# Optimization experiments

Hardware: AMD Instinct MI355X
Metric: run time of the kernel (lower is better)

The kernel has to match this reference:

```python
import jax, jax.numpy as jnp
import numpy as np

N, IN_FT, OUT_FT = 10000, 512, 256


def setup_inputs() -> dict:
    key = jax.random.key(0)
    k1, k2, k3 = jax.random.split(key, 3)
    feat = jax.random.normal(k1, (N, IN_FT), dtype=jnp.float32)
    adj = jax.random.uniform(k2, (N, N), dtype=jnp.float32)  # nonneg edge weights
    W = jax.random.normal(k3, (IN_FT, OUT_FT), dtype=jnp.float32) * 0.05
    conv_bias = jnp.zeros((OUT_FT,), dtype=jnp.float32)
    extra_bias = jnp.zeros((OUT_FT,), dtype=jnp.float32)
    return {"feat": feat, "adj": adj, "W": W,
            "conv_bias": conv_bias, "extra_bias": extra_bias}


def reference(feat, adj, W, conv_bias, extra_bias):
    n = adj.shape[0]
    idx = jnp.arange(n)
    # gcn_norm: fill_diag(adj, 1.0) -> self loops with weight 1 on the diagonal
    A_hat = adj.at[idx, idx].set(1.0)  # [N, N]
    deg = A_hat.sum(axis=1)            # row degree
    dinv = jnp.where(deg > 0, jax.lax.rsqrt(deg), 0.0)  # D^-1/2
    # linear transform first (standard GCNConv order), then normalized aggregation
    h = feat @ W                                   # [N, OUT_FT]
    # D^-1/2 A_hat D^-1/2 h, fused as row/col scalings to avoid a second NxN buffer
    agg = dinv[:, None] * (A_hat @ (dinv[:, None] * h))
    out = agg + conv_bias + extra_bias
    return jax.nn.relu(out)
```

## Files before the change

### kernel.cpp

```cpp
#include <hip/hip_runtime.h>

#define NROW 10000
#define NF 256
#define KF 512
#define MP 10048
#define NTILES 157

typedef __attribute__((ext_vector_type(8))) short short8x;
typedef __attribute__((ext_vector_type(4))) float f32x4;

__device__ __forceinline__ unsigned int bf16rne(float f){
  unsigned int u = __builtin_bit_cast(unsigned int, f);
  u += 0x7fffu + ((u >> 16) & 1u);
  return u >> 16;
}

__global__ void k_zero(float4* __restrict__ p){
  p[blockIdx.x * 256 + threadIdx.x] = make_float4(0.f, 0.f, 0.f, 0.f);
}

__global__ __launch_bounds__(256) void k_deg2(const float* __restrict__ adj,
        float* __restrict__ degp){
  int t = threadIdx.x;
  int lane = t & 63;
  int row = blockIdx.x * 4 + (t >> 6);
  const f32x4* src = (const f32x4*)(adj + (size_t)row * NROW);
  const f32x4 zero4 = {0.f, 0.f, 0.f, 0.f};
  f32x4 acc0 = zero4, acc1 = zero4;
  f32x4 v[8];
  #pragma unroll
  for (int it = 0; it < 4; ++it){
    int base = it * 512 + lane;
    #pragma unroll
    for (int b = 0; b < 8; ++b) v[b] = src[base + b * 64];
    #pragma unroll
    for (int b = 0; b < 4; ++b){ acc0 += v[2*b]; acc1 += v[2*b + 1]; }
  }
  {
    int base = 2048 + lane;
    #pragma unroll
    for (int b = 0; b < 8; ++b){
      int fi = base + b * 64;
      v[b] = (fi < 2500) ? src[fi] : zero4;
    }
    #pragma unroll
    for (int b = 0; b < 4; ++b){ acc0 += v[2*b]; acc1 += v[2*b + 1]; }
  }
  f32x4 a = acc0 + acc1;
  float s = (a[0] + a[1]) + (a[2] + a[3]);
  #pragma unroll
  for (int off = 32; off; off >>= 1) s += __shfl_down(s, off);
  if (lane == 0) degp[row] = s;
}

__global__ void k_dinv(const float* __restrict__ degp, const float* __restrict__ adj,
                       float* __restrict__ dinv, unsigned short* __restrict__ hsT){
  int i = blockIdx.x * 256 + threadIdx.x;
  if (i >= MP) return;
  float d = 0.f;
  if (i < NROW){
    float tot = degp[i] + 1.0f - adj[(size_t)i * NROW + i];
    d = tot > 0.f ? rsqrtf(tot) : 0.f;
  }
  dinv[i] = d;
  if (i < NF){
    unsigned int* tz = (unsigned int*)(hsT + (size_t)i * MP + NROW);
    #pragma unroll
    for (int m = 0; m < (MP - NROW) / 2; ++m) tz[m] = 0u;
  }
}

__global__ __launch_bounds__(128) void k_featw(const float* __restrict__ feat,
        const float* __restrict__ W, const float* __restrict__ dinv,
        unsigned short* __restrict__ hsT){
  __shared__ __align__(16) float fs[8][512];
  int t = threadIdx.x;
  int i0 = blockIdx.x * 8;
  #pragma unroll
  for (int it = 0; it < 8; ++it){
    int idx = it * 128 + t;
    int r = idx >> 7, c4 = (idx & 127) * 4;
    *(float4*)&fs[r][c4] = *(const float4*)(feat + (size_t)(i0 + r) * KF + c4);
  }
  __syncthreads();
  float acc[8][2];
  #pragma unroll
  for (int r = 0; r < 8; ++r){ acc[r][0] = 0.f; acc[r][1] = 0.f; }
  int c0 = t, c1 = t + 128;
  for (int k = 0; k < KF; k += 4){
    const float* Wk = W + (size_t)k * NF;
    float w0a = Wk[c0],        w0b = Wk[c1];
    float w1a = Wk[NF + c0],   w1b = Wk[NF + c1];
    float w2a = Wk[2*NF + c0], w2b = Wk[2*NF + c1];
    float w3a = Wk[3*NF + c0], w3b = Wk[3*NF + c1];
    #pragma unroll
    for (int r = 0; r < 8; ++r){
      float4 f = *(const float4*)&fs[r][k];
      float a0 = acc[r][0], a1 = acc[r][1];
      a0 = fmaf(f.x, w0a, a0); a1 = fmaf(f.x, w0b, a1);
      a0 = fmaf(f.y, w1a, a0); a1 = fmaf(f.y, w1b, a1);
      a0 = fmaf(f.z, w2a, a0); a1 = fmaf(f.z, w2b, a1);
      a0 = fmaf(f.w, w3a, a0); a1 = fmaf(f.w, w3b, a1);
      acc[r][0] = a0; acc[r][1] = a1;
    }
  }
  float dv[8];
  #pragma unroll
  for (int r = 0; r < 8; ++r) dv[r] = dinv[i0 + r];
  unsigned short* d0 = hsT + (size_t)c0 * MP + i0;
  unsigned short* d1 = hsT + (size_t)c1 * MP + i0;
  #pragma unroll
  for (int r = 0; r < 8; r += 2){
    unsigned int u0 = bf16rne(acc[r][0] * dv[r]) | (bf16rne(acc[r+1][0] * dv[r+1]) << 16);
    unsigned int u1 = bf16rne(acc[r][1] * dv[r]) | (bf16rne(acc[r+1][1] * dv[r+1]) << 16);
    *(unsigned int*)(d0 + r) = u0;
    *(unsigned int*)(d1 + r) = u1;
  }
}

__global__ __launch_bounds__(256, 2) void k_gemm(const float* __restrict__ adj,
        const unsigned short* __restrict__ hsT, float* __restrict__ out){
  __shared__ __align__(16) unsigned short Al[64][72];
  __shared__ __align__(16) unsigned short Bl[256][72];
  int t = threadIdx.x;
  int lane = t & 63, wid = t >> 6;
  int wr = wid >> 1, wc = wid & 1;
  int r0 = blockIdx.x * 64;
  int by = blockIdx.y;
  int kt0 = by * 39 + (by > 0 ? 1 : 0);
  int kt1 = (by + 1) * 39 + 1;

  f32x4 acc[2][8];
  #pragma unroll
  for (int a = 0; a < 2; ++a)
    #pragma unroll
    for (int b = 0; b < 8; ++b)
      #pragma unroll
      for (int j = 0; j < 4; ++j) acc[a][b][j] = 0.f;

  int arow = t >> 4;
  int acol = (t & 15) * 4;
  int bcol = t >> 3;
  int bko  = (t & 7) * 8;

  for (int kt = kt0; kt < kt1; ++kt){
    int k0 = kt * 64;
    #pragma unroll
    for (int it = 0; it < 4; ++it){
      int row = it * 16 + arow;
      int gr  = r0 + row;
      int gcb = k0 + acol;
      int er = gr  < NROW      ? gr  : NROW - 1;
      int ec = gcb <= NROW - 4 ? gcb : NROW - 4;
      float4 v = *(const float4*)(adj + (size_t)er * NROW + ec);
      float f0 = v.x, f1 = v.y, f2 = v.z, f3 = v.w;
      if (gr == gcb    ) f0 = 1.f;
      if (gr == gcb + 1) f1 = 1.f;
      if (gr == gcb + 2) f2 = 1.f;
      if (gr == gcb + 3) f3 = 1.f;
      unsigned int u0 = bf16rne(f0) | (bf16rne(f1) << 16);
      unsigned int u1 = bf16rne(f2) | (bf16rne(f3) << 16);
      *(uint2*)&Al[row][acol] = make_uint2(u0, u1);
    }
    #pragma unroll
    for (int it = 0; it < 8; ++it){
      int cc = it * 32 + bcol;
      *(uint4*)&Bl[cc][bko] = *(const uint4*)(hsT + (size_t)cc * MP + k0 + bko);
    }
    __syncthreads();
    #pragma unroll
    for (int kk = 0; kk < 64; kk += 32){
      short8x a0 = *(const short8x*)&Al[wr*32      + (lane & 15)][kk + (lane >> 4) * 8];
      short8x a1 = *(const short8x*)&Al[wr*32 + 16 + (lane & 15)][kk + (lane >> 4) * 8];
      #pragma unroll
      for (int ni = 0; ni < 8; ++ni){
        short8x b = *(const short8x*)&Bl[wc*128 + ni*16 + (lane & 15)][kk + (lane >> 4) * 8];
        acc[0][ni] = __builtin_amdgcn_mfma_f32_16x16x32_bf16(a0, b, acc[0][ni], 0, 0, 0);
        acc[1][ni] = __builtin_amdgcn_mfma_f32_16x16x32_bf16(a1, b, acc[1][ni], 0, 0, 0);
      }
    }
    __syncthreads();
  }
  #pragma unroll
  for (int mi = 0; mi < 2; ++mi){
    #pragma unroll
    for (int ni = 0; ni < 8; ++ni){
      int gc = wc*128 + ni*16 + (lane & 15);
      #pragma unroll
      for (int j = 0; j < 4; ++j){
        int gr = r0 + wr*32 + mi*16 + (lane >> 4) * 4 + j;
        if (gr < NROW) atomicAdd(out + (size_t)gr * NF + gc, acc[mi][ni][j]);
      }
    }
  }
}

__global__ void k_epi(float* __restrict__ out, const float* __restrict__ dinv,
                      const float* __restrict__ cb, const float* __restrict__ eb){
  int e = (blockIdx.x * 256 + threadIdx.x) * 4;
  int i = e >> 8, c = e & 255;
  float di = dinv[i];
  float4 v = *(float4*)(out + e);
  v.x = fmaxf(fmaf(v.x, di, cb[c+0] + eb[c+0]), 0.f);
  v.y = fmaxf(fmaf(v.y, di, cb[c+1] + eb[c+1]), 0.f);
  v.z = fmaxf(fmaf(v.z, di, cb[c+2] + eb[c+2]), 0.f);
  v.w = fmaxf(fmaf(v.w, di, cb[c+3] + eb[c+3]), 0.f);
  *(float4*)(out + e) = v;
}

extern "C" void kernel_launch(void* const* d_in, const int* in_sizes, int n_in,
                              void* d_out, int out_size, void* d_ws, size_t ws_size,
                              hipStream_t stream){
  const float* feat = (const float*)d_in[0];
  const float* adj  = (const float*)d_in[1];
  const float* W    = (const float*)d_in[2];
  const float* cb   = (const float*)d_in[3];
  const float* eb   = (const float*)d_in[4];
  float* out = (float*)d_out;

  float* degp = (float*)d_ws;
  float* dinv = (float*)((char*)d_ws + (256u << 10));
  unsigned short* hsT = (unsigned short*)((char*)d_ws + (512u << 10));

  k_zero <<<(NROW*NF)/1024,   256, 0, stream>>>((float4*)out);
  k_deg2 <<<NROW/4,           256, 0, stream>>>(adj, degp);
  k_dinv <<<(MP + 255)/256,   256, 0, stream>>>(degp, adj, dinv, hsT);
  k_featw<<<NROW/8,           128, 0, stream>>>(feat, W, dinv, hsT);
  k_gemm <<<dim3(NTILES, 4),  256, 0, stream>>>(adj, hsT, out);
  k_epi  <<<(NROW*NF)/1024,   256, 0, stream>>>(out, dinv, cb, eb);
}
```

Baseline: 279.0 us.

## Drop B shared-memory staging, read hsT directly from global with wider K tiles

The GEMM kernel no longer stages the transposed h tile in LDS. Each lane loads its bf16 B fragments straight from global/L2, and only the adjacency tile is staged, now 256 wide in K per iteration instead of 64. This cuts LDS traffic and halves the number of barriers per K element, and the smaller LDS footprint plus launch_bounds 4 allow more resident blocks. In exchange, B fragments are re-read from cache by every wave, and the padded K length grows to 10240, which adds extra zero work.

```diff
diff --git a/kernel.cpp b/kernel.cpp
--- a/kernel.cpp
+++ b/kernel.cpp
@@ -3,7 +3,8 @@
 #define NROW 10000
 #define NF 256
 #define KF 512
-#define MP 10048
+#define MPK 10240
+#define NKT 40
 #define NTILES 157
 
 typedef __attribute__((ext_vector_type(8))) short short8x;
@@ -56,17 +57,17 @@
 __global__ void k_dinv(const float* __restrict__ degp, const float* __restrict__ adj,
                        float* __restrict__ dinv, unsigned short* __restrict__ hsT){
   int i = blockIdx.x * 256 + threadIdx.x;
-  if (i >= MP) return;
+  if (i >= MPK) return;
   float d = 0.f;
   if (i < NROW){
     float tot = degp[i] + 1.0f - adj[(size_t)i * NROW + i];
     d = tot > 0.f ? rsqrtf(tot) : 0.f;
   }
-  dinv[i] = d;
+  if (i < MPK) dinv[i] = d;
   if (i < NF){
-    unsigned int* tz = (unsigned int*)(hsT + (size_t)i * MP + NROW);
-    #pragma unroll
-    for (int m = 0; m < (MP - NROW) / 2; ++m) tz[m] = 0u;
+    unsigned int* tz = (unsigned int*)(hsT + (size_t)i * MPK + NROW);
+    #pragma unroll
+    for (int m = 0; m < (MPK - NROW) / 2; ++m) tz[m] = 0u;
   }
 }
 
@@ -107,8 +108,8 @@
   float dv[8];
   #pragma unroll
   for (int r = 0; r < 8; ++r) dv[r] = dinv[i0 + r];
-  unsigned short* d0 = hsT + (size_t)c0 * MP + i0;
-  unsigned short* d1 = hsT + (size_t)c1 * MP + i0;
+  unsigned short* d0 = hsT + (size_t)c0 * MPK + i0;
+  unsigned short* d1 = hsT + (size_t)c1 * MPK + i0;
   #pragma unroll
   for (int r = 0; r < 8; r += 2){
     unsigned int u0 = bf16rne(acc[r][0] * dv[r]) | (bf16rne(acc[r+1][0] * dv[r+1]) << 16);
@@ -118,17 +119,16 @@
   }
 }
 
-__global__ __launch_bounds__(256, 2) void k_gemm(const float* __restrict__ adj,
+__global__ __launch_bounds__(256, 4) void k_gemm(const float* __restrict__ adj,
         const unsigned short* __restrict__ hsT, float* __restrict__ out){
-  __shared__ __align__(16) unsigned short Al[64][72];
-  __shared__ __align__(16) unsigned short Bl[256][72];
+  __shared__ __align__(16) unsigned short Al[64][264];
   int t = threadIdx.x;
   int lane = t & 63, wid = t >> 6;
   int wr = wid >> 1, wc = wid & 1;
+  int l15 = lane & 15, hi = lane >> 4;
   int r0 = blockIdx.x * 64;
-  int by = blockIdx.y;
-  int kt0 = by * 39 + (by > 0 ? 1 : 0);
-  int kt1 = (by + 1) * 39 + 1;
+  int kt0 = blockIdx.y * (NKT/4);
+  int kt1 = kt0 + (NKT/4);
 
   f32x4 acc[2][8];
   #pragma unroll
@@ -138,43 +138,42 @@
       #pragma unroll
       for (int j = 0; j < 4; ++j) acc[a][b][j] = 0.f;
 
-  int arow = t >> 4;
-  int acol = (t & 15) * 4;
-  int bcol = t >> 3;
-  int bko  = (t & 7) * 8;
+  int srow = t >> 4;
+  int scol = (t & 15) * 4;
+  const unsigned short* bbase = hsT + (size_t)(wc*128 + l15) * MPK;
 
   for (int kt = kt0; kt < kt1; ++kt){
-    int k0 = kt * 64;
+    int k0 = kt * 256;
     #pragma unroll
     for (int it = 0; it < 4; ++it){
-      int row = it * 16 + arow;
+      int row = it * 16 + srow;
       int gr  = r0 + row;
-      int gcb = k0 + acol;
-      int er = gr  < NROW      ? gr  : NROW - 1;
-      int ec = gcb <= NROW - 4 ? gcb : NROW - 4;
-      float4 v = *(const float4*)(adj + (size_t)er * NROW + ec);
-      float f0 = v.x, f1 = v.y, f2 = v.z, f3 = v.w;
-      if (gr == gcb    ) f0 = 1.f;
-      if (gr == gcb + 1) f1 = 1.f;
-      if (gr == gcb + 2) f2 = 1.f;
-      if (gr == gcb + 3) f3 = 1.f;
-      unsigned int u0 = bf16rne(f0) | (bf16rne(f1) << 16);
-      unsigned int u1 = bf16rne(f2) | (bf16rne(f3) << 16);
-      *(uint2*)&Al[row][acol] = make_uint2(u0, u1);
-    }
-    #pragma unroll
-    for (int it = 0; it < 8; ++it){
-      int cc = it * 32 + bcol;
-      *(uint4*)&Bl[cc][bko] = *(const uint4*)(hsT + (size_t)cc * MP + k0 + bko);
+      int er  = gr < NROW ? gr : NROW - 1;
+      const float* rowp = adj + (size_t)er * NROW;
+      #pragma unroll
+      for (int j = 0; j < 4; ++j){
+        int gcb = k0 + scol + j * 64;
+        int ec  = gcb <= NROW - 4 ? gcb : NROW - 4;
+        float4 v = *(const float4*)(rowp + ec);
+        float f0 = v.x, f1 = v.y, f2 = v.z, f3 = v.w;
+        if (gr == gcb    ) f0 = 1.f;
+        if (gr == gcb + 1) f1 = 1.f;
+        if (gr == gcb + 2) f2 = 1.f;
+        if (gr == gcb + 3) f3 = 1.f;
+        unsigned int u0 = bf16rne(f0) | (bf16rne(f1) << 16);
+        unsigned int u1 = bf16rne(f2) | (bf16rne(f3) << 16);
+        *(uint2*)&Al[row][scol + j * 64] = make_uint2(u0, u1);
+      }
     }
     __syncthreads();
     #pragma unroll
-    for (int kk = 0; kk < 64; kk += 32){
-      short8x a0 = *(const short8x*)&Al[wr*32      + (lane & 15)][kk + (lane >> 4) * 8];
-      short8x a1 = *(const short8x*)&Al[wr*32 + 16 + (lane & 15)][kk + (lane >> 4) * 8];
+    for (int k8 = 0; k8 < 8; ++k8){
+      short8x a0 = *(const short8x*)&Al[wr*32      + l15][k8*32 + hi*8];
+      short8x a1 = *(const short8x*)&Al[wr*32 + 16 + l15][k8*32 + hi*8];
+      const unsigned short* bk = bbase + k0 + k8*32 + hi*8;
       #pragma unroll
       for (int ni = 0; ni < 8; ++ni){
-        short8x b = *(const short8x*)&Bl[wc*128 + ni*16 + (lane & 15)][kk + (lane >> 4) * 8];
+        short8x b = *(const short8x*)(bk + (size_t)ni * 16 * MPK);
         acc[0][ni] = __builtin_amdgcn_mfma_f32_16x16x32_bf16(a0, b, acc[0][ni], 0, 0, 0);
         acc[1][ni] = __builtin_amdgcn_mfma_f32_16x16x32_bf16(a1, b, acc[1][ni], 0, 0, 0);
       }
@@ -185,10 +184,10 @@
   for (int mi = 0; mi < 2; ++mi){
     #pragma unroll
     for (int ni = 0; ni < 8; ++ni){
-      int gc = wc*128 + ni*16 + (lane & 15);
+      int gc = wc*128 + ni*16 + l15;
       #pragma unroll
       for (int j = 0; j < 4; ++j){
-        int gr = r0 + wr*32 + mi*16 + (lane >> 4) * 4 + j;
+        int gr = r0 + wr*32 + mi*16 + hi*4 + j;
         if (gr < NROW) atomicAdd(out + (size_t)gr * NF + gc, acc[mi][ni][j]);
       }
     }
@@ -224,7 +223,7 @@
 
   k_zero <<<(NROW*NF)/1024,   256, 0, stream>>>((float4*)out);
   k_deg2 <<<NROW/4,           256, 0, stream>>>(adj, degp);
-  k_dinv <<<(MP + 255)/256,   256, 0, stream>>>(degp, adj, dinv, hsT);
+  k_dinv <<<(MPK + 255)/256,  256, 0, stream>>>(degp, adj, dinv, hsT);
   k_featw<<<NROW/8,           128, 0, stream>>>(feat, W, dinv, hsT);
   k_gemm <<<dim3(NTILES, 4),  256, 0, stream>>>(adj, hsT, out);
   k_epi  <<<(NROW*NF)/1024,   256, 0, stream>>>(out, dinv, cb, eb);
```

Result: slower. 470.4 us (+68.6%).

## Double-buffer adj tiles via direct global-to-LDS loads and replace atomics with split-K partials

Applied to the files above, without the earlier changes.

The GEMM kernel now streams fp32 adjacency tiles straight into swizzled LDS with global_load_lds, double-buffered so the next tile loads while the current one is computed. The bf16 conversion moves to fragment-read time, and the per-element diagonal fix-up is dropped from the inner loop. The epilogue instead adds the self-loop correction (1 - a_ii)·h_i. Atomic adds into a zeroed output are replaced by four split-K partial buffers that the epilogue sums, which also removes the zero kernel. This costs extra workspace traffic for the partials and doubles the LDS footprint for A.

```diff
diff --git a/kernel.cpp b/kernel.cpp
--- a/kernel.cpp
+++ b/kernel.cpp
@@ -4,6 +4,7 @@
 #define NF 256
 #define KF 512
 #define MP 10048
+#define NKT 157
 #define NTILES 157
 
 typedef __attribute__((ext_vector_type(8))) short short8x;
@@ -14,9 +15,14 @@
   u += 0x7fffu + ((u >> 16) & 1u);
   return u >> 16;
 }
-
-__global__ void k_zero(float4* __restrict__ p){
-  p[blockIdx.x * 256 + threadIdx.x] = make_float4(0.f, 0.f, 0.f, 0.f);
+__device__ __forceinline__ float bf2f(unsigned short h){
+  unsigned int u = ((unsigned int)h) << 16;
+  return __builtin_bit_cast(float, u);
+}
+__device__ __forceinline__ void gload16(const void* g, void* l){
+  __builtin_amdgcn_global_load_lds(
+      (const __attribute__((address_space(1))) unsigned int*)g,
+      (__attribute__((address_space(3))) unsigned int*)l, 16, 0, 0);
 }
 
 __global__ __launch_bounds__(256) void k_deg2(const float* __restrict__ adj,
@@ -119,16 +125,18 @@
 }
 
 __global__ __launch_bounds__(256, 2) void k_gemm(const float* __restrict__ adj,
-        const unsigned short* __restrict__ hsT, float* __restrict__ out){
-  __shared__ __align__(16) unsigned short Al[64][72];
+        const unsigned short* __restrict__ hsT, float* __restrict__ part){
+  __shared__ __align__(16) float Afs[2][4096];
   __shared__ __align__(16) unsigned short Bl[256][72];
   int t = threadIdx.x;
   int lane = t & 63, wid = t >> 6;
   int wr = wid >> 1, wc = wid & 1;
+  int l15 = lane & 15, hi = lane >> 4;
   int r0 = blockIdx.x * 64;
   int by = blockIdx.y;
   int kt0 = by * 39 + (by > 0 ? 1 : 0);
   int kt1 = (by + 1) * 39 + 1;
+  int ktf = kt1 < NKT ? kt1 : NKT - 1;
 
   f32x4 acc[2][8];
   #pragma unroll
@@ -138,74 +146,145 @@
       #pragma unroll
       for (int j = 0; j < 4; ++j) acc[a][b][j] = 0.f;
 
-  int arow = t >> 4;
-  int acol = (t & 15) * 4;
+  const float* asrc[4];
+  int adstoff[4];
+  {
+    int srow = (wid << 2) + hi;
+    #pragma unroll
+    for (int j = 0; j < 4; ++j){
+      int row = j * 16 + srow;
+      int gr  = r0 + row;
+      int er  = gr < NROW ? gr : NROW - 1;
+      int logf = ((l15 * 16) ^ ((row & 7) << 4)) >> 2;
+      asrc[j] = adj + (size_t)er * NROW + logf;
+      adstoff[j] = (j * 4096 + wid * 1024 + lane * 16) >> 2;
+    }
+  }
   int bcol = t >> 3;
   int bko  = (t & 7) * 8;
 
-  for (int kt = kt0; kt < kt1; ++kt){
+  #define STAGE_A(buf, k0g) { \
+    _Pragma("unroll") \
+    for (int j = 0; j < 4; ++j) \
+      gload16(asrc[j] + (k0g), &Afs[buf][adstoff[j]]); }
+
+  #define LDA_FRAG(dst, buf, rowv, kk) { \
+    int row_ = (rowv); \
+    int sw_  = (row_ & 7) << 4; \
+    const char* rp_ = (const char*)&Afs[buf][row_ * 64]; \
+    int b0_ = (kk) * 128 + hi * 32; \
+    f32x4 lo_ = *(const f32x4*)(rp_ + ((b0_     ) ^ sw_)); \
+    f32x4 hh_ = *(const f32x4*)(rp_ + ((b0_ + 16) ^ sw_)); \
+    union { unsigned int u[4]; short8x s; } cv_; \
+    cv_.u[0] = bf16rne(lo_[0]) | (bf16rne(lo_[1]) << 16); \
+    cv_.u[1] = bf16rne(lo_[2]) | (bf16rne(lo_[3]) << 16); \
+    cv_.u[2] = bf16rne(hh_[0]) | (bf16rne(hh_[1]) << 16); \
+    cv_.u[3] = bf16rne(hh_[2]) | (bf16rne(hh_[3]) << 16); \
+    dst = cv_.s; }
+
+  #define COMPUTE(buf) { \
+    _Pragma("unroll") \
+    for (int kk = 0; kk < 2; ++kk){ \
+      short8x a0_, a1_; \
+      LDA_FRAG(a0_, buf, wr*32      + l15, kk); \
+      LDA_FRAG(a1_, buf, wr*32 + 16 + l15, kk); \
+      _Pragma("unroll") \
+      for (int ni = 0; ni < 8; ++ni){ \
+        short8x b_ = *(const short8x*)&Bl[wc*128 + ni*16 + l15][kk*32 + hi*8]; \
+        acc[0][ni] = __builtin_amdgcn_mfma_f32_16x16x32_bf16(a0_, b_, acc[0][ni], 0, 0, 0); \
+        acc[1][ni] = __builtin_amdgcn_mfma_f32_16x16x32_bf16(a1_, b_, acc[1][ni], 0, 0, 0); \
+      } \
+    } }
+
+  int cur = 0;
+  STAGE_A(0, kt0 * 64);
+  for (int kt = kt0; kt < ktf; ++kt){
     int k0 = kt * 64;
-    #pragma unroll
-    for (int it = 0; it < 4; ++it){
-      int row = it * 16 + arow;
-      int gr  = r0 + row;
-      int gcb = k0 + acol;
-      int er = gr  < NROW      ? gr  : NROW - 1;
-      int ec = gcb <= NROW - 4 ? gcb : NROW - 4;
-      float4 v = *(const float4*)(adj + (size_t)er * NROW + ec);
-      float f0 = v.x, f1 = v.y, f2 = v.z, f3 = v.w;
-      if (gr == gcb    ) f0 = 1.f;
-      if (gr == gcb + 1) f1 = 1.f;
-      if (gr == gcb + 2) f2 = 1.f;
-      if (gr == gcb + 3) f3 = 1.f;
-      unsigned int u0 = bf16rne(f0) | (bf16rne(f1) << 16);
-      unsigned int u1 = bf16rne(f2) | (bf16rne(f3) << 16);
-      *(uint2*)&Al[row][acol] = make_uint2(u0, u1);
-    }
-    #pragma unroll
-    for (int it = 0; it < 8; ++it){
-      int cc = it * 32 + bcol;
-      *(uint4*)&Bl[cc][bko] = *(const uint4*)(hsT + (size_t)cc * MP + k0 + bko);
-    }
+    uint4 bb[8];
+    #pragma unroll
+    for (int it = 0; it < 8; ++it)
+      bb[it] = *(const uint4*)(hsT + (size_t)(it*32 + bcol) * MP + k0 + bko);
+    __builtin_amdgcn_sched_barrier(0);
+    if (kt + 1 < ktf) STAGE_A(cur ^ 1, k0 + 64);
+    __builtin_amdgcn_sched_barrier(0);
+    #pragma unroll
+    for (int it = 0; it < 8; ++it)
+      *(uint4*)&Bl[it*32 + bcol][bko] = bb[it];
+    asm volatile("s_waitcnt lgkmcnt(0)\ns_barrier" ::: "memory");
+    COMPUTE(cur);
+    asm volatile("s_barrier" ::: "memory");
+    cur ^= 1;
+  }
+  if (kt1 == NKT){
+    int k0 = (NKT - 1) * 64;
+    #pragma unroll
+    for (int s4 = 0; s4 < 4; ++s4){
+      int slot = s4 * 256 + t;
+      int row = slot >> 4;
+      int physb = (slot & 15) * 16;
+      int logb  = physb ^ ((row & 7) << 4);
+      int gr = r0 + row;
+      int er = gr < NROW ? gr : NROW - 1;
+      int gc = k0 + (logb >> 2);
+      int ec = gc <= NROW - 4 ? gc : NROW - 4;
+      f32x4 v = *(const f32x4*)(adj + (size_t)er * NROW + ec);
+      *(f32x4*)((char*)&Afs[cur][row * 64] + physb) = v;
+    }
+    #pragma unroll
+    for (int it = 0; it < 8; ++it)
+      *(uint4*)&Bl[it*32 + bcol][bko] =
+          *(const uint4*)(hsT + (size_t)(it*32 + bcol) * MP + k0 + bko);
     __syncthreads();
-    #pragma unroll
-    for (int kk = 0; kk < 64; kk += 32){
-      short8x a0 = *(const short8x*)&Al[wr*32      + (lane & 15)][kk + (lane >> 4) * 8];
-      short8x a1 = *(const short8x*)&Al[wr*32 + 16 + (lane & 15)][kk + (lane >> 4) * 8];
-      #pragma unroll
-      for (int ni = 0; ni < 8; ++ni){
-        short8x b = *(const short8x*)&Bl[wc*128 + ni*16 + (lane & 15)][kk + (lane >> 4) * 8];
-        acc[0][ni] = __builtin_amdgcn_mfma_f32_16x16x32_bf16(a0, b, acc[0][ni], 0, 0, 0);
-        acc[1][ni] = __builtin_amdgcn_mfma_f32_16x16x32_bf16(a1, b, acc[1][ni], 0, 0, 0);
-      }
-    }
-    __syncthreads();
-  }
+    COMPUTE(cur);
+  }
+  float* pb = part + (size_t)by * ((size_t)MP * NF);
   #pragma unroll
   for (int mi = 0; mi < 2; ++mi){
     #pragma unroll
     for (int ni = 0; ni < 8; ++ni){
-      int gc = wc*128 + ni*16 + (lane & 15);
+      int gc = wc*128 + ni*16 + l15;
       #pragma unroll
       for (int j = 0; j < 4; ++j){
-        int gr = r0 + wr*32 + mi*16 + (lane >> 4) * 4 + j;
-        if (gr < NROW) atomicAdd(out + (size_t)gr * NF + gc, acc[mi][ni][j]);
+        int gr = r0 + wr*32 + mi*16 + hi*4 + j;
+        if (gr < NROW) pb[(size_t)gr * NF + gc] = acc[mi][ni][j];
       }
     }
   }
-}
-
-__global__ void k_epi(float* __restrict__ out, const float* __restrict__ dinv,
-                      const float* __restrict__ cb, const float* __restrict__ eb){
+  #undef STAGE_A
+  #undef LDA_FRAG
+  #undef COMPUTE
+}
+
+__global__ void k_epi(const float* __restrict__ part, const float* __restrict__ adj,
+                      const unsigned short* __restrict__ hsT,
+                      const float* __restrict__ dinv, const float* __restrict__ cb,
+                      const float* __restrict__ eb, float* __restrict__ out){
   int e = (blockIdx.x * 256 + threadIdx.x) * 4;
   int i = e >> 8, c = e & 255;
+  const size_t PS = (size_t)MP * NF;
+  size_t o = (size_t)i * NF + c;
+  float4 s0 = *(const float4*)(part + o);
+  float4 s1 = *(const float4*)(part + PS + o);
+  float4 s2 = *(const float4*)(part + 2*PS + o);
+  float4 s3 = *(const float4*)(part + 3*PS + o);
+  float sx = (s0.x + s1.x) + (s2.x + s3.x);
+  float sy = (s0.y + s1.y) + (s2.y + s3.y);
+  float sz = (s0.z + s1.z) + (s2.z + s3.z);
+  float sw = (s0.w + s1.w) + (s2.w + s3.w);
+  float aii = adj[(size_t)i * NROW + i];
+  float av  = __builtin_bit_cast(float, bf16rne(aii) << 16);
+  float w   = 1.0f - av;
+  sx += w * bf2f(hsT[(size_t)(c+0) * MP + i]);
+  sy += w * bf2f(hsT[(size_t)(c+1) * MP + i]);
+  sz += w * bf2f(hsT[(size_t)(c+2) * MP + i]);
+  sw += w * bf2f(hsT[(size_t)(c+3) * MP + i]);
   float di = dinv[i];
-  float4 v = *(float4*)(out + e);
-  v.x = fmaxf(fmaf(v.x, di, cb[c+0] + eb[c+0]), 0.f);
-  v.y = fmaxf(fmaf(v.y, di, cb[c+1] + eb[c+1]), 0.f);
-  v.z = fmaxf(fmaf(v.z, di, cb[c+2] + eb[c+2]), 0.f);
-  v.w = fmaxf(fmaf(v.w, di, cb[c+3] + eb[c+3]), 0.f);
-  *(float4*)(out + e) = v;
+  float4 r;
+  r.x = fmaxf(fmaf(sx, di, cb[c+0] + eb[c+0]), 0.f);
+  r.y = fmaxf(fmaf(sy, di, cb[c+1] + eb[c+1]), 0.f);
+  r.z = fmaxf(fmaf(sz, di, cb[c+2] + eb[c+2]), 0.f);
+  r.w = fmaxf(fmaf(sw, di, cb[c+3] + eb[c+3]), 0.f);
+  *(float4*)(out + e) = r;
 }
 
 extern "C" void kernel_launch(void* const* d_in, const int* in_sizes, int n_in,
@@ -221,11 +300,11 @@
   float* degp = (float*)d_ws;
   float* dinv = (float*)((char*)d_ws + (256u << 10));
   unsigned short* hsT = (unsigned short*)((char*)d_ws + (512u << 10));
-
-  k_zero <<<(NROW*NF)/1024,   256, 0, stream>>>((float4*)out);
+  float* part = (float*)((char*)d_ws + (8u << 20));
+
   k_deg2 <<<NROW/4,           256, 0, stream>>>(adj, degp);
   k_dinv <<<(MP + 255)/256,   256, 0, stream>>>(degp, adj, dinv, hsT);
   k_featw<<<NROW/8,           128, 0, stream>>>(feat, W, dinv, hsT);
-  k_gemm <<<dim3(NTILES, 4),  256, 0, stream>>>(adj, hsT, out);
-  k_epi  <<<(NROW*NF)/1024,   256, 0, stream>>>(out, dinv, cb, eb);
-}
+  k_gemm <<<dim3(NTILES, 4),  256, 0, stream>>>(adj, hsT, part);
+  k_epi  <<<(NROW*NF)/1024,   256, 0, stream>>>(part, adj, hsT, dinv, cb, eb, out);
+}
```

New measurement: 318.3 us. 1.14x slower.
